# Kernel optimization log

Measured on AMD Instinct MI355X. Metric: run time of the kernel, lower is better.

Reference implementation:

```python
import jax, jax.numpy as jnp
import numpy as np

PAD = 2  # matches init_kwargs padding

# HEALPix face layout (DLWP-HEALPix / earth2grid convention):
#   faces 0-3 : northern polar cap
#   faces 4-7 : equatorial belt
#   faces 8-11: southern polar cap
# Padding each face gathers edge strips from topological neighbor faces;
# polar-cap neighbors require 90/180-degree rotations, and the two degenerate
# equatorial corners (touching a pole vertex, 3 faces meet) are filled with
# edge continuations + an averaged corner pixel.

def _rot(x, k):
    return jnp.rot90(x, k, axes=(-2, -1))

def _corner_tl(t, l, p):
    # degenerate top-left corner of an equatorial face (pole vertex)
    shp = t.shape[:-2] + (p, p)
    c = jnp.zeros(shp, t.dtype)
    c = c.at[..., :, -1].set(t[..., -p:, 0])          # continue top neighbor's left edge
    c = c.at[..., -1, :].set(l[..., 0, -p:])          # continue left neighbor's top edge
    c = c.at[..., -1, -1].set(0.5 * t[..., -1, 0] + 0.5 * l[..., 0, -1])
    return c

def _corner_br(b, r, p):
    # degenerate bottom-right corner of an equatorial face (pole vertex)
    shp = b.shape[:-2] + (p, p)
    c = jnp.zeros(shp, b.dtype)
    c = c.at[..., :, 0].set(b[..., :p, -1])
    c = c.at[..., 0, :].set(r[..., -1, :p])
    c = c.at[..., 0, 0].set(0.5 * b[..., 0, -1] + 0.5 * r[..., -1, 0])
    return c

def _assemble(tl, t, tr, l, c, r, bl, b, br):
    top = jnp.concatenate([tl, t, tr], axis=-1)
    mid = jnp.concatenate([l, c, r], axis=-1)
    bot = jnp.concatenate([bl, b, br], axis=-1)
    return jnp.concatenate([top, mid, bot], axis=-2)

def _pn(c, t, tl, l, bl, b, br, r, tr, p):
    # northern polar face: top/left neighbors are rotated polar faces
    return _assemble(
        _rot(tl, 2)[..., -p:, -p:], _rot(t, 1)[..., -p:, :], _rot(tr, 1)[..., -p:, :p],
        _rot(l, -1)[..., :, -p:],   c,                       r[..., :, :p],
        bl[..., :p, -p:],           b[..., :p, :],           br[..., :p, :p])

def _pe(c, t, tl, l, bl, b, br, r, tr, p):
    # equatorial face: no rotations; tl/br are precomputed degenerate corners
    return _assemble(
        tl,               t[..., -p:, :], tr[..., -p:, :p],
        l[..., :, -p:],   c,              r[..., :, :p],
        bl[..., :p, -p:], b[..., :p, :],  br)

def _ps(c, t, tl, l, bl, b, br, r, tr, p):
    # southern polar face: mirror image of the northern case
    return _assemble(
        tl[..., -p:, :p], t[..., -p:, :],        tr[..., -p:, -p:],
        l[..., :, -p:],   c,                     _rot(r, -1)[..., :, :p],
        _rot(bl, 1)[..., :p, -p:], _rot(b, 1)[..., :p, :], _rot(br, 2)[..., :p, :p])

def healpix_pad(x, p):
    # x: (B, 12, C, H, W) -> (B, 12, C, H+2p, W+2p)
    f = [x[:, i] for i in range(12)]
    out = []
    for i in range(4):  # northern cap faces 0..3
        out.append(_pn(f[i], t=f[(i + 1) % 4], tl=f[(i + 2) % 4], l=f[(i - 1) % 4],
                       bl=f[(i - 1) % 4], b=f[4 + i], br=f[8 + i],
                       r=f[4 + (i + 1) % 4], tr=f[(i + 1) % 4], p=p))
    for i in range(4):  # equatorial faces 4..7
        out.append(_pe(f[4 + i], t=f[i], tl=_corner_tl(f[i], f[(i - 1) % 4], p),
                       l=f[(i - 1) % 4], bl=f[4 + (i - 1) % 4], b=f[8 + i],
                       br=_corner_br(f[8 + i], f[8 + (i - 1) % 4], p),
                       r=f[4 + (i + 1) % 4], tr=f[i], p=p))
    for i in range(4):  # southern cap faces 8..11
        out.append(_ps(f[8 + i], t=f[4 + i], tl=f[4 + i], l=f[4 + (i + 1) % 4],
                       bl=f[8 + (i + 1) % 4], b=f[8 + (i - 1) % 4], br=f[8 + (i - 1) % 4],
                       r=f[8 + (i + 1) % 4], tr=f[i], p=p))
    return jnp.stack(out, axis=1)


def setup_inputs() -> dict:
    key = jax.random.key(0)
    x = jax.random.normal(key, (2, 12, 32, 256, 256), dtype=jnp.float32)
    return {"x": x}


def reference(x) -> jnp.ndarray:
    return healpix_pad(x, PAD)
```

## Files before the change

### kernel.cpp

```cpp
#include <hip/hip_runtime.h>


constexpr int N  = 256;
constexpr int P  = 2;
constexpr int NP = N + 2 * P;
constexpr int C  = 32;
constexpr int PLANE_OUT = NP * NP;
constexpr int PLANE_IN  = N * N;

typedef float f32x4 __attribute__((ext_vector_type(4)));

__device__ __forceinline__ float gather(const float* __restrict__ in,
                                        int basePlane, int face, int i,
                                        int oh, int ow) {
    auto L = [&](int f, int sh, int sw) -> float {
        return in[(size_t)(basePlane + f * C) * PLANE_IN + sh * N + sw];
    };

    float v;
    if (face < 4) {
        if (oh < P) {
            if (ow < P)              v = L((i + 2) & 3, P - 1 - oh, P - 1 - ow);
            else if (ow < P + N)     v = L((i + 1) & 3, ow - P, P - 1 - oh);
            else                     v = L((i + 1) & 3, ow - P - N, P - 1 - oh);
        } else if (oh < P + N) {
            int ch = oh - P;
            if (ow < P)              v = L((i + 3) & 3, P - 1 - ow, ch);
            else if (ow < P + N)     v = L(face, ch, ow - P);
            else                     v = L(4 + ((i + 1) & 3), ch, ow - P - N);
        } else {
            int bh = oh - P - N;
            if (ow < P)              v = L((i + 3) & 3, bh, N - P + ow);
            else if (ow < P + N)     v = L(4 + i, bh, ow - P);
            else                     v = L(8 + i, bh, ow - P - N);
        }
    } else if (face < 8) {
        if (oh < P) {
            if (ow < P) {
                if (oh == P - 1 && ow == P - 1)
                    v = 0.5f * L(i, N - 1, 0) + 0.5f * L((i + 3) & 3, 0, N - 1);
                else if (oh == P - 1) v = L((i + 3) & 3, 0, N - P + ow);
                else if (ow == P - 1) v = L(i, N - P + oh, 0);
                else                  v = 0.0f;
            }
            else if (ow < P + N)     v = L(i, N - P + oh, ow - P);
            else                     v = L(i, N - P + oh, ow - P - N);
        } else if (oh < P + N) {
            int ch = oh - P;
            if (ow < P)              v = L((i + 3) & 3, ch, N - P + ow);
            else if (ow < P + N)     v = L(face, ch, ow - P);
            else                     v = L(4 + ((i + 1) & 3), ch, ow - P - N);
        } else {
            int bh = oh - P - N;
            if (ow < P)              v = L(4 + ((i + 3) & 3), bh, N - P + ow);
            else if (ow < P + N)     v = L(8 + i, bh, ow - P);
            else {
                int bw = ow - P - N;
                if (bh == 0 && bw == 0)
                    v = 0.5f * L(8 + i, 0, N - 1) + 0.5f * L(8 + ((i + 3) & 3), N - 1, 0);
                else if (bh == 0)     v = L(8 + ((i + 3) & 3), N - 1, bw);
                else if (bw == 0)     v = L(8 + i, bh, N - 1);
                else                  v = 0.0f;
            }
        }
    } else {
        if (oh < P) {
            if (ow < P)              v = L(4 + i, N - P + oh, ow);
            else if (ow < P + N)     v = L(4 + i, N - P + oh, ow - P);
            else                     v = L(i, N - P + oh, N - P + (ow - P - N));
        } else if (oh < P + N) {
            int ch = oh - P;
            if (ow < P)              v = L(4 + ((i + 1) & 3), ch, N - P + ow);
            else if (ow < P + N)     v = L(face, ch, ow - P);
            else {
                int bw = ow - P - N;
                v = L(8 + ((i + 1) & 3), N - 1 - bw, ch);
            }
        } else {
            int bh = oh - P - N;
            if (ow < P)              v = L(8 + ((i + 1) & 3), N - P + ow, N - 1 - bh);
            else if (ow < P + N)     v = L(8 + ((i + 3) & 3), ow - P, N - 1 - bh);
            else {
                int bw = ow - P - N;
                v = L(8 + ((i + 3) & 3), N - 1 - bh, N - 1 - bw);
            }
        }
    }
    return v;
}

__global__ __launch_bounds__(256)
void healpix_pad_kernel(const float* __restrict__ in, float* __restrict__ out) {
    const int plane = blockIdx.y;
    const int g     = blockIdx.x * 4 + (threadIdx.x >> 6);
    if (g > 64) return;
    const int l     = threadIdx.x & 63;

    float* __restrict__ oplane = out + (size_t)plane * PLANE_OUT;
    const float* __restrict__ iplane = in + (size_t)plane * PLANE_IN;

    const int bc   = plane >> 5;
    const int face = bc >= 12 ? bc - 12 : bc;
    const int i    = face & 3;
    const int basePlane = plane - face * C;
    const int r0   = g * 4;

    #pragma unroll
    for (int it = 0; it < 5; ++it) {
        const int c = it * 64 + l;
        if (c >= 260) break;
        const int q   = c / 65;
        const int j   = c - q * 65;
        const int row = r0 + q;
        const int ow  = 4 * j;

        f32x4 v;
        if (row >= P && row < P + N) {
            const float* __restrict__ src = iplane + (row - P) * N;
            if (j == 0) {
                v.x = gather(in, basePlane, face, i, row, 0);
                v.y = gather(in, basePlane, face, i, row, 1);
                float2 a = *reinterpret_cast<const float2*>(src);
                v.z = a.x; v.w = a.y;
            } else if (j == 64) {
                float2 b = *reinterpret_cast<const float2*>(src + N - 2);
                v.x = b.x; v.y = b.y;
                v.z = gather(in, basePlane, face, i, row, NP - 2);
                v.w = gather(in, basePlane, face, i, row, NP - 1);
            } else {
                float2 a = *reinterpret_cast<const float2*>(src + ow - 2);
                float2 b = *reinterpret_cast<const float2*>(src + ow);
                v = f32x4{a.x, a.y, b.x, b.y};
            }
        } else {
            v.x = gather(in, basePlane, face, i, row, ow);
            v.y = gather(in, basePlane, face, i, row, ow + 1);
            v.z = gather(in, basePlane, face, i, row, ow + 2);
            v.w = gather(in, basePlane, face, i, row, ow + 3);
        }
        __builtin_nontemporal_store(v, reinterpret_cast<f32x4*>(oplane + row * NP + ow));
    }
}

extern "C" void kernel_launch(void* const* d_in, const int* in_sizes, int n_in,
                              void* d_out, int out_size, void* d_ws, size_t ws_size,
                              hipStream_t stream) {
    const float* in = (const float*)d_in[0];
    float* out = (float*)d_out;
    int planes = out_size / PLANE_OUT;
    dim3 block(256);
    dim3 grid(17, planes);
    healpix_pad_kernel<<<grid, block, 0, stream>>>(in, out);
}
```

Before: 72.15 us.

## Prefetch interior loads into registers and stage halo edges in shared memory

```diff
diff --git a/kernel.cpp b/kernel.cpp
--- a/kernel.cpp
+++ b/kernel.cpp
@@ -91,52 +91,82 @@
 
 __global__ __launch_bounds__(256)
 void healpix_pad_kernel(const float* __restrict__ in, float* __restrict__ out) {
+    __shared__ float edges[16][4];
+    __shared__ __align__(16) float rowbuf[2][NP];
+
     const int plane = blockIdx.y;
-    const int g     = blockIdx.x * 4 + (threadIdx.x >> 6);
-    if (g > 64) return;
-    const int l     = threadIdx.x & 63;
-
-    float* __restrict__ oplane = out + (size_t)plane * PLANE_OUT;
-    const float* __restrict__ iplane = in + (size_t)plane * PLANE_IN;
+    const int bx    = blockIdx.x;
+    const int tid   = threadIdx.x;
+    const int w     = tid >> 6;
+    const int l     = tid & 63;
+    const int s     = bx * 4 + w;
 
     const int bc   = plane >> 5;
     const int face = bc >= 12 ? bc - 12 : bc;
-    const int i    = face & 3;
+    const int fi   = face & 3;
     const int basePlane = plane - face * C;
-    const int r0   = g * 4;
+    const float* __restrict__ iplane = in + (size_t)plane * PLANE_IN;
+    float* __restrict__ oplane = out + (size_t)plane * PLANE_OUT;
+
+    const int r0 = s * 4;
+    float2 A[5], B[5];
+    if (s <= 64) {
+        #pragma unroll
+        for (int it = 0; it < 5; ++it) {
+            int c = it * 64 + l; if (c > 259) c = 259;
+            int q = c / 65, j = c - q * 65;
+            int row = r0 + q;
+            int ir  = row - P;
+            ir = ir < 0 ? 0 : (ir > 255 ? 255 : ir);
+            const float* src = iplane + ir * N;
+            int off1 = (j == 0) ? 0 : (4 * j - 2);
+            int off2 = (j >= 64) ? 252 : 4 * j;
+            A[it] = *reinterpret_cast<const float2*>(src + off1);
+            B[it] = *reinterpret_cast<const float2*>(src + off2);
+        }
+    }
+
+    if (tid < 64) {
+        int row = bx * 16 + (tid >> 2);
+        if (row >= P && row <= 257) {
+            int e  = tid & 3;
+            int ow = (e < 2) ? e : 256 + e;
+            edges[tid >> 2][e] = gather(in, basePlane, face, fi, row, ow);
+        }
+    }
+    if (bx == 0 || bx == 16) {
+        for (int t = tid; t < 2 * NP; t += 256) {
+            int r01 = t >= NP ? 1 : 0;
+            int col = t - NP * r01;
+            int oh  = (bx == 0) ? r01 : 258 + r01;
+            rowbuf[r01][col] = gather(in, basePlane, face, fi, oh, col);
+        }
+    }
+    __syncthreads();
+
+    if (s > 64) return;
 
     #pragma unroll
     for (int it = 0; it < 5; ++it) {
-        const int c = it * 64 + l;
-        if (c >= 260) break;
-        const int q   = c / 65;
-        const int j   = c - q * 65;
-        const int row = r0 + q;
-        const int ow  = 4 * j;
+        int c = it * 64 + l;
+        if (c > 259) continue;
+        int q = c / 65, j = c - q * 65;
+        int row = r0 + q;
+        int ow  = 4 * j;
 
         f32x4 v;
-        if (row >= P && row < P + N) {
-            const float* __restrict__ src = iplane + (row - P) * N;
-            if (j == 0) {
-                v.x = gather(in, basePlane, face, i, row, 0);
-                v.y = gather(in, basePlane, face, i, row, 1);
-                float2 a = *reinterpret_cast<const float2*>(src);
-                v.z = a.x; v.w = a.y;
-            } else if (j == 64) {
-                float2 b = *reinterpret_cast<const float2*>(src + N - 2);
-                v.x = b.x; v.y = b.y;
-                v.z = gather(in, basePlane, face, i, row, NP - 2);
-                v.w = gather(in, basePlane, face, i, row, NP - 1);
-            } else {
-                float2 a = *reinterpret_cast<const float2*>(src + ow - 2);
-                float2 b = *reinterpret_cast<const float2*>(src + ow);
-                v = f32x4{a.x, a.y, b.x, b.y};
-            }
+        if (row < P || row > 257) {
+            int rb = row < P ? row : row - 258;
+            v = *reinterpret_cast<const f32x4*>(&rowbuf[rb][ow]);
         } else {
-            v.x = gather(in, basePlane, face, i, row, ow);
-            v.y = gather(in, basePlane, face, i, row, ow + 1);
-            v.z = gather(in, basePlane, face, i, row, ow + 2);
-            v.w = gather(in, basePlane, face, i, row, ow + 3);
+            int rl = row - bx * 16;
+            float e0 = edges[rl][0], e1 = edges[rl][1];
+            float e2 = edges[rl][2], e3 = edges[rl][3];
+            float x  = (j == 0) ? e0 : A[it].x;
+            float y  = (j == 0) ? e1 : A[it].y;
+            float z  = (j == 0) ? A[it].x : ((j == 64) ? e2 : B[it].x);
+            float wv = (j == 0) ? A[it].y : ((j == 64) ? e3 : B[it].y);
+            v = f32x4{x, y, z, wv};
         }
         __builtin_nontemporal_store(v, reinterpret_cast<f32x4*>(oplane + row * NP + ow));
     }
```

Result: faster. 70.59 us, median of 2 (-2.2%).
